# Kernel optimization log

Hardware: AMD Instinct MI355X
Metric: run time of the kernel (lower is better)

The kernel has to match this reference:

```python
import jax, jax.numpy as jnp
import numpy as np
from jax import lax

# Production-scale dims: batch, seq_len, tag_size (incl. START/STOP tags)
B, S, T = 512, 512, 64


def setup_inputs() -> dict:
    key = jax.random.key(0)
    k1, k2, k3, k4 = jax.random.split(key, 4)
    feats = jax.random.normal(k1, (B, S, T), dtype=jnp.float32)
    # prefix-contiguous mask (module assumes mask[:, 0] == 1 and length-style masks)
    lengths = jax.random.randint(k2, (B,), S // 2, S + 1)
    mask = jnp.arange(S)[None, :] < lengths[:, None]  # (B, S) bool
    tags = jax.random.randint(k3, (B, S), 0, T - 2)  # gold tags exclude START/STOP
    transitions = jax.random.normal(k4, (T, T), dtype=jnp.float32) * 0.1
    return {"feats": feats, "mask": mask, "tags": tags, "transitions": transitions}


def _crf_nll(feats, transitions, mask, tags):
    b, s, t = feats.shape
    START, STOP = t - 2, t - 1  # START_TAG = -2, STOP_TAG = -1

    # ---- forward (log partition), matches _calculate_PZ ----
    # partition init: scores[0][:, START, :] = feats[:,0,:] + transitions[START, :]
    init = feats[:, 0, :] + transitions[START][None, :]  # (b, t)

    feats_t = jnp.swapaxes(feats, 0, 1)  # (s, b, t)
    mask_t = jnp.swapaxes(mask, 0, 1)    # (s, b)

    def step(partition, inp):
        f_t, m_t = inp  # (b, t), (b,)
        # cur_values[b, from, to] = feats_t[b, to] + transitions[from, to] + partition[b, from]
        cur = partition[:, :, None] + transitions[None, :, :] + f_t[:, None, :]
        new_p = jax.nn.logsumexp(cur, axis=1)  # reduce over 'from' -> (b, t)
        partition = jnp.where(m_t[:, None], new_p, partition)
        return partition, None

    partition, _ = lax.scan(step, init, (feats_t[1:], mask_t[1:]))

    # final transition to STOP
    final = jax.nn.logsumexp(partition[:, :, None] + transitions[None, :, :], axis=1)
    forward_score = final[:, STOP].sum()

    # ---- gold score, matches _score_sentence ----
    prev = jnp.concatenate(
        [jnp.full((b, 1), START, dtype=tags.dtype), tags[:, :-1]], axis=1
    )  # (b, s): previous tag, START at position 0
    emit = jnp.take_along_axis(feats, tags[:, :, None], axis=2)[:, :, 0]  # (b, s)
    tg_energy = emit + transitions[prev, tags]  # (b, s)
    gold = jnp.where(mask, tg_energy, jnp.zeros((), feats.dtype)).sum()
    lengths = mask.sum(axis=1).astype(jnp.int32)  # (b,)
    end_ids = jnp.take_along_axis(tags, (lengths - 1)[:, None].astype(tags.dtype), axis=1)[:, 0]
    gold = gold + transitions[end_ids, STOP].sum()

    # average_batch = False
    return forward_score - gold


def reference(feats, mask, tags, transitions):
    return _crf_nll(feats, transitions, mask, tags)
```

## Files before the change

kernel.cpp:

```cpp
#include <hip/hip_runtime.h>

#define BB 512
#define SS 512
#define TT 64
#define START_TAG 62
#define STOP_TAG 63

#define LOG2E 1.4426950408889634f
#define LN2   0.6931471805599453f

typedef _Float16 h2 __attribute__((ext_vector_type(2)));
typedef _Float16 h8 __attribute__((ext_vector_type(8)));
typedef float    f4 __attribute__((ext_vector_type(4)));

__device__ __forceinline__ h2 pkrtz(float a, float b) {
    return __builtin_bit_cast(h2, __builtin_amdgcn_cvt_pkrtz(a, b));
}
__device__ __forceinline__ f4 MF(h8 a, h8 b, f4 c) {
    return __builtin_amdgcn_mfma_f32_16x16x32_f16(a, b, c, 0, 0, 0);
}

__global__ void __launch_bounds__(192) crf_main(
    const float* __restrict__ feats, const int* __restrict__ mask,
    const int* __restrict__ tags, const float* __restrict__ trans,
    float* __restrict__ out)
{
    const int b    = blockIdx.x;
    const int tid  = threadIdx.x;
    const int wv   = tid >> 6;
    const int lane = tid & 63;

    const float* frow = feats + (size_t)b * SS * TT;
    const int*   mrow = mask + b * SS;

    __shared__ __align__(16) _Float16 febuf[2][8][TT];
    __shared__ __align__(16) float xbuf[TT];
    __shared__ __align__(16) float ybuf[TT];
    __shared__ int ks_sh;

    int cnt = 0;
    #pragma unroll
    for (int s = lane; s < SS; s += 64) cnt += (mrow[s] != 0);
    #pragma unroll
    for (int off = 32; off; off >>= 1) cnt += __shfl_xor(cnt, off);
    const int len = cnt;
    const int h   = len >> 1;

    float offs = 0.f;
    int   ksum = 0;

    if (wv < 2) {
        const bool isF = (wv == 0);
        const int g  = lane >> 4;
        const int cg = lane & 15;
        const int to_base = 16 * (cg >> 2) + (cg & 3);
        const int nstep = isF ? h : (len - h - 2);
        const int base  = isF ? 1 : (len - 2);
        const int dir   = isF ? 1 : -1;
        _Float16 (*febw)[TT] = febuf[wv];

        h8 A[4][2];
        #pragma unroll
        for (int tt = 0; tt < 4; ++tt)
            #pragma unroll
            for (int kc = 0; kc < 2; ++kc)
                #pragma unroll
                for (int j = 0; j < 8; ++j) {
                    const int kt = 16 * g + 8 * kc + j;
                    const int ot = to_base + 4 * tt;
                    const int ix = isF ? (kt * TT + ot) : (ot * TT + kt);
                    A[tt][kc][j] =
                        (_Float16)__builtin_amdgcn_exp2f(trans[ix] * LOG2E);
                }

        h8 B0, B1;
        if (isF) {
            offs = frow[0] + trans[START_TAG * TT + 0];
            #pragma unroll
            for (int sl = 0; sl < 8; ++sl) {
                const int t0 = 16 * g + sl, t1 = t0 + 8;
                B0[sl] = (_Float16)__builtin_amdgcn_exp2f(
                    (frow[t0] + trans[START_TAG * TT + t0] - offs) * LOG2E);
                B1[sl] = (_Float16)__builtin_amdgcn_exp2f(
                    (frow[t1] + trans[START_TAG * TT + t1] - offs) * LOG2E);
            }
        } else {
            const float* fl = frow + (size_t)(len - 1) * TT;
            #pragma unroll
            for (int sl = 0; sl < 8; ++sl) {
                const int t0 = 16 * g + sl, t1 = t0 + 8;
                B0[sl] = (_Float16)__builtin_amdgcn_exp2f(
                    (fl[t0] + trans[t0 * TT + STOP_TAG]) * LOG2E);
                B1[sl] = (_Float16)__builtin_amdgcn_exp2f(
                    (fl[t1] + trans[t1 * TT + STOP_TAG]) * LOG2E);
            }
        }

        auto rowOf = [&](int idx) {
            int r = base + dir * idx;
            return r < 0 ? 0 : (r > SS - 1 ? SS - 1 : r);
        };

        float fr[8];
        #pragma unroll
        for (int j = 0; j < 8; ++j)
            fr[j] = frow[(size_t)rowOf(j) * TT + lane];
        #pragma unroll
        for (int j = 0; j < 4; ++j)
            febw[rowOf(j) & 7][lane] =
                (_Float16)__builtin_amdgcn_exp2f(fr[j] * LOG2E);
        h8 cL0, cL1, cL2, cL3, cH0, cH1, cH2, cH3;
        {
            const _Float16* p0 = &febw[rowOf(0) & 7][16 * g];
            const _Float16* p1 = &febw[rowOf(1) & 7][16 * g];
            const _Float16* p2 = &febw[rowOf(2) & 7][16 * g];
            const _Float16* p3 = &febw[rowOf(3) & 7][16 * g];
            cL0 = *(const h8*)p0; cH0 = *(const h8*)(p0 + 8);
            cL1 = *(const h8*)p1; cH1 = *(const h8*)(p1 + 8);
            cL2 = *(const h8*)p2; cH2 = *(const h8*)(p2 + 8);
            cL3 = *(const h8*)p3; cH3 = *(const h8*)(p3 + 8);
        }

        const f4 Z = {0.f, 0.f, 0.f, 0.f};
        auto STEP = [&](h8 feL, h8 feH) {
            f4 d0 = MF(A[0][0], B0, Z);
            f4 d1 = MF(A[1][0], B0, Z);
            f4 d2 = MF(A[2][0], B0, Z);
            f4 d3 = MF(A[3][0], B0, Z);
            d0 = MF(A[0][1], B1, d0);
            d1 = MF(A[1][1], B1, d1);
            d2 = MF(A[2][1], B1, d2);
            d3 = MF(A[3][1], B1, d3);
            const int eb = (__builtin_amdgcn_readfirstlane(
                                __float_as_int(d0[0])) >> 23) & 0xff;
            ksum += eb - 127;
            const float sc = __int_as_float((254 - eb) << 23);
            const h2 p0 = pkrtz(d0[0] * sc, d0[1] * sc);
            const h2 p1 = pkrtz(d0[2] * sc, d0[3] * sc);
            const h2 p2 = pkrtz(d1[0] * sc, d1[1] * sc);
            const h2 p3 = pkrtz(d1[2] * sc, d1[3] * sc);
            const h2 p4 = pkrtz(d2[0] * sc, d2[1] * sc);
            const h2 p5 = pkrtz(d2[2] * sc, d2[3] * sc);
            const h2 p6 = pkrtz(d3[0] * sc, d3[1] * sc);
            const h2 p7 = pkrtz(d3[2] * sc, d3[3] * sc);
            const h2 q0 = p0 * __builtin_shufflevector(feL, feL, 0, 1);
            const h2 q1 = p1 * __builtin_shufflevector(feL, feL, 2, 3);
            const h2 q2 = p2 * __builtin_shufflevector(feL, feL, 4, 5);
            const h2 q3 = p3 * __builtin_shufflevector(feL, feL, 6, 7);
            const h2 q4 = p4 * __builtin_shufflevector(feH, feH, 0, 1);
            const h2 q5 = p5 * __builtin_shufflevector(feH, feH, 2, 3);
            const h2 q6 = p6 * __builtin_shufflevector(feH, feH, 4, 5);
            const h2 q7 = p7 * __builtin_shufflevector(feH, feH, 6, 7);
            B0 = __builtin_shufflevector(
                     __builtin_shufflevector(q0, q1, 0, 1, 2, 3),
                     __builtin_shufflevector(q2, q3, 0, 1, 2, 3),
                     0, 1, 2, 3, 4, 5, 6, 7);
            B1 = __builtin_shufflevector(
                     __builtin_shufflevector(q4, q5, 0, 1, 2, 3),
                     __builtin_shufflevector(q6, q7, 0, 1, 2, 3),
                     0, 1, 2, 3, 4, 5, 6, 7);
        };

        int i = 0;
        for (; i + 3 < nstep; i += 4) {
            const float n0 = frow[(size_t)rowOf(i + 8)  * TT + lane];
            const float n1 = frow[(size_t)rowOf(i + 9)  * TT + lane];
            const float n2 = frow[(size_t)rowOf(i + 10) * TT + lane];
            const float n3 = frow[(size_t)rowOf(i + 11) * TT + lane];
            febw[rowOf(i + 4) & 7][lane] =
                (_Float16)__builtin_amdgcn_exp2f(fr[4] * LOG2E);
            febw[rowOf(i + 5) & 7][lane] =
                (_Float16)__builtin_amdgcn_exp2f(fr[5] * LOG2E);
            febw[rowOf(i + 6) & 7][lane] =
                (_Float16)__builtin_amdgcn_exp2f(fr[6] * LOG2E);
            febw[rowOf(i + 7) & 7][lane] =
                (_Float16)__builtin_amdgcn_exp2f(fr[7] * LOG2E);
            const _Float16* q0p = &febw[rowOf(i + 4) & 7][16 * g];
            const _Float16* q1p = &febw[rowOf(i + 5) & 7][16 * g];
            const _Float16* q2p = &febw[rowOf(i + 6) & 7][16 * g];
            const _Float16* q3p = &febw[rowOf(i + 7) & 7][16 * g];
            const h8 nL0 = *(const h8*)q0p, nH0 = *(const h8*)(q0p + 8);
            const h8 nL1 = *(const h8*)q1p, nH1 = *(const h8*)(q1p + 8);
            const h8 nL2 = *(const h8*)q2p, nH2 = *(const h8*)(q2p + 8);
            const h8 nL3 = *(const h8*)q3p, nH3 = *(const h8*)(q3p + 8);

            STEP(cL0, cH0); STEP(cL1, cH1); STEP(cL2, cH2); STEP(cL3, cH3);

            cL0 = nL0; cH0 = nH0; cL1 = nL1; cH1 = nH1;
            cL2 = nL2; cH2 = nH2; cL3 = nL3; cH3 = nH3;
            #pragma unroll
            for (int j = 0; j < 4; ++j) fr[j] = fr[j + 4];
            fr[4] = n0; fr[5] = n1; fr[6] = n2; fr[7] = n3;
        }

        const int rem = nstep - i;
        if (rem > 0) STEP(cL0, cH0);
        if (rem > 1) STEP(cL1, cH1);
        if (rem > 2) STEP(cL2, cH2);

        if (isF) {
            f4 d0 = MF(A[0][0], B0, Z);
            f4 d1 = MF(A[1][0], B0, Z);
            f4 d2 = MF(A[2][0], B0, Z);
            f4 d3 = MF(A[3][0], B0, Z);
            d0 = MF(A[0][1], B1, d0);
            d1 = MF(A[1][1], B1, d1);
            d2 = MF(A[2][1], B1, d2);
            d3 = MF(A[3][1], B1, d3);
            const int eb = (__builtin_amdgcn_readfirstlane(
                                __float_as_int(d0[0])) >> 23) & 0xff;
            ksum += eb - 127;
            const float sc = __int_as_float((254 - eb) << 23);
            if (cg == 0) {
                #pragma unroll
                for (int r = 0; r < 4; ++r) {
                    xbuf[16 * g + 0 * 4 + r] = d0[r] * sc;
                    xbuf[16 * g + 1 * 4 + r] = d1[r] * sc;
                    xbuf[16 * g + 2 * 4 + r] = d2[r] * sc;
                    xbuf[16 * g + 3 * 4 + r] = d3[r] * sc;
                }
            }
        } else {
            if (cg == 0) {
                #pragma unroll
                for (int sl = 0; sl < 8; ++sl) {
                    ybuf[16 * g + sl]     = (float)B0[sl];
                    ybuf[16 * g + 8 + sl] = (float)B1[sl];
                }
            }
            if (lane == 0) ks_sh = ksum;
        }
    } else {
        const int* trow = tags + b * SS;
        float acc = 0.f;
        for (int s = lane; s < SS; s += 64) {
            if (mrow[s] != 0) {
                const int tag  = trow[s];
                const int prev = (s == 0) ? START_TAG : trow[s - 1];
                acc += frow[(size_t)s * TT + tag] + trans[prev * TT + tag];
            }
        }
        #pragma unroll
        for (int off = 32; off; off >>= 1) acc += __shfl_xor(acc, off);
        if (lane == 0) {
            const int end_id = trow[len - 1];
            atomicAdd(out, -(acc + trans[end_id * TT + STOP_TAG]));
        }
    }

    __syncthreads();

    if (wv == 0) {
        float z = xbuf[lane] * ybuf[lane];
        #pragma unroll
        for (int off = 32; off; off >>= 1) z += __shfl_xor(z, off);
        if (lane == 0)
            atomicAdd(out, offs + (float)(ksum + ks_sh) * LN2
                           + LN2 * __builtin_amdgcn_logf(z));
    }
}

extern "C" void kernel_launch(void* const* d_in, const int* in_sizes, int n_in,
                              void* d_out, int out_size, void* d_ws, size_t ws_size,
                              hipStream_t stream) {
    const float* feats = (const float*)d_in[0];
    const int*   mask  = (const int*)d_in[1];
    const int*   tags  = (const int*)d_in[2];
    const float* trans = (const float*)d_in[3];
    float* out = (float*)d_out;

    (void)hipMemsetAsync(out, 0, sizeof(float), stream);
    crf_main<<<BB, 192, 0, stream>>>(feats, mask, tags, trans, out);
}
```

Before: 166.8 us.

## Split CRF recurrence into four segments using transfer-matrix products on extra waves

Sequential forward-algorithm work goes from two chains (forward and backward halves) to four segments. Two extra waves each accumulate a 64x64 product of per-step transfer matrices with MFMA for a middle segment, and the results are combined through shared memory at the end. The aim is a shorter serial critical path per block. In exchange each matrix-step costs four times the MFMAs of a vector step, occupancy per block rises to 256 threads, and a small fp32 matrix-vector epilogue is added. The per-step fp16 rescaling of the whole matrix by a single exponent risks precision loss.

Result: slower. 215.0 us (+28.9%).

```diff
diff --git a/kernel.cpp b/kernel.cpp
--- a/kernel.cpp
+++ b/kernel.cpp
@@ -20,7 +20,7 @@
     return __builtin_amdgcn_mfma_f32_16x16x32_f16(a, b, c, 0, 0, 0);
 }
 
-__global__ void __launch_bounds__(192) crf_main(
+__global__ void __launch_bounds__(256) crf_main(
     const float* __restrict__ feats, const int* __restrict__ mask,
     const int* __restrict__ tags, const float* __restrict__ trans,
     float* __restrict__ out)
@@ -29,14 +29,17 @@
     const int tid  = threadIdx.x;
     const int wv   = tid >> 6;
     const int lane = tid & 63;
+    const int g    = lane >> 4;
+    const int cg   = lane & 15;
 
     const float* frow = feats + (size_t)b * SS * TT;
     const int*   mrow = mask + b * SS;
 
-    __shared__ __align__(16) _Float16 febuf[2][8][TT];
-    __shared__ __align__(16) float xbuf[TT];
-    __shared__ __align__(16) float ybuf[TT];
-    __shared__ int ks_sh;
+    __shared__ __align__(16) _Float16 febuf[4][8][TT];
+    __shared__ __align__(16) _Float16 TAbuf[TT][TT];
+    __shared__ __align__(16) _Float16 TBbuf[TT][TT];
+    __shared__ __align__(16) float xbuf[TT], ubuf[TT], x2buf[TT];
+    __shared__ int ks_sh[4];
 
     int cnt = 0;
     #pragma unroll
@@ -44,37 +47,87 @@
     #pragma unroll
     for (int off = 32; off; off >>= 1) cnt += __shfl_xor(cnt, off);
     const int len = cnt;
-    const int h   = len >> 1;
+
+    int h1 = (len >> 2) - 9;
+    const int remt = len - 2 - h1;
+    const int mA = remt / 3, mB = remt / 3;
 
     float offs = 0.f;
     int   ksum = 0;
 
-    if (wv < 2) {
-        const bool isF = (wv == 0);
-        const int g  = lane >> 4;
-        const int cg = lane & 15;
-        const int to_base = 16 * (cg >> 2) + (cg & 3);
-        const int nstep = isF ? h : (len - h - 2);
-        const int base  = isF ? 1 : (len - 2);
-        const int dir   = isF ? 1 : -1;
-        _Float16 (*febw)[TT] = febuf[wv];
-
-        h8 A[4][2];
-        #pragma unroll
-        for (int tt = 0; tt < 4; ++tt)
-            #pragma unroll
-            for (int kc = 0; kc < 2; ++kc)
-                #pragma unroll
-                for (int j = 0; j < 8; ++j) {
-                    const int kt = 16 * g + 8 * kc + j;
-                    const int ot = to_base + 4 * tt;
-                    const int ix = isF ? (kt * TT + ot) : (ot * TT + kt);
-                    A[tt][kc][j] =
-                        (_Float16)__builtin_amdgcn_exp2f(trans[ix] * LOG2E);
-                }
-
+    if (wv == 0) {
+        const int* trow = tags + b * SS;
+        float acc = 0.f;
+        for (int s = lane; s < SS; s += 64) {
+            if (mrow[s] != 0) {
+                const int tag  = trow[s];
+                const int prev = (s == 0) ? START_TAG : trow[s - 1];
+                acc += frow[(size_t)s * TT + tag] + trans[prev * TT + tag];
+            }
+        }
+        #pragma unroll
+        for (int off = 32; off; off >>= 1) acc += __shfl_xor(acc, off);
+        if (lane == 0) {
+            const int end_id = trow[len - 1];
+            atomicAdd(out, -(acc + trans[end_id * TT + STOP_TAG]));
+        }
+    }
+
+    const bool isB   = (wv == 1);
+    const bool isMat = (wv >= 2);
+    const int nstep = (wv == 0) ? h1
+                    : (wv == 1) ? (remt - mA - mB)
+                    : (wv == 2) ? mA : mB;
+    const int base  = (wv == 0) ? 1
+                    : (wv == 1) ? (len - 2)
+                    : (wv == 2) ? (h1 + 1) : (h1 + mA + 1);
+    const int dir   = isB ? -1 : 1;
+    _Float16 (*febw)[TT] = febuf[wv];
+
+    const int to_base = 16 * (cg >> 2) + (cg & 3);
+    h8 A[4][2];
+    #pragma unroll
+    for (int tt = 0; tt < 4; ++tt)
+        #pragma unroll
+        for (int kc = 0; kc < 2; ++kc)
+            #pragma unroll
+            for (int j = 0; j < 8; ++j) {
+                const int kt = 16 * g + 8 * kc + j;
+                const int ot = to_base + 4 * tt;
+                const int ix = isB ? (ot * TT + kt) : (kt * TT + ot);
+                A[tt][kc][j] =
+                    (_Float16)__builtin_amdgcn_exp2f(trans[ix] * LOG2E);
+            }
+
+    auto rowOf = [&](int idx) {
+        int r = base + dir * idx;
+        return r < 0 ? 0 : (r > SS - 1 ? SS - 1 : r);
+    };
+
+    float fr[8];
+    #pragma unroll
+    for (int j = 0; j < 8; ++j)
+        fr[j] = frow[(size_t)rowOf(j) * TT + lane];
+    #pragma unroll
+    for (int j = 0; j < 4; ++j)
+        febw[rowOf(j) & 7][lane] =
+            (_Float16)__builtin_amdgcn_exp2f(fr[j] * LOG2E);
+    h8 cL0, cL1, cL2, cL3, cH0, cH1, cH2, cH3;
+    {
+        const _Float16* p0 = &febw[rowOf(0) & 7][16 * g];
+        const _Float16* p1 = &febw[rowOf(1) & 7][16 * g];
+        const _Float16* p2 = &febw[rowOf(2) & 7][16 * g];
+        const _Float16* p3 = &febw[rowOf(3) & 7][16 * g];
+        cL0 = *(const h8*)p0; cH0 = *(const h8*)(p0 + 8);
+        cL1 = *(const h8*)p1; cH1 = *(const h8*)(p1 + 8);
+        cL2 = *(const h8*)p2; cH2 = *(const h8*)(p2 + 8);
+        cL3 = *(const h8*)p3; cH3 = *(const h8*)(p3 + 8);
+    }
+    const f4 Zz = {0.f, 0.f, 0.f, 0.f};
+
+    if (!isMat) {
         h8 B0, B1;
-        if (isF) {
+        if (wv == 0) {
             offs = frow[0] + trans[START_TAG * TT + 0];
             #pragma unroll
             for (int sl = 0; sl < 8; ++sl) {
@@ -96,37 +149,11 @@
             }
         }
 
-        auto rowOf = [&](int idx) {
-            int r = base + dir * idx;
-            return r < 0 ? 0 : (r > SS - 1 ? SS - 1 : r);
-        };
-
-        float fr[8];
-        #pragma unroll
-        for (int j = 0; j < 8; ++j)
-            fr[j] = frow[(size_t)rowOf(j) * TT + lane];
-        #pragma unroll
-        for (int j = 0; j < 4; ++j)
-            febw[rowOf(j) & 7][lane] =
-                (_Float16)__builtin_amdgcn_exp2f(fr[j] * LOG2E);
-        h8 cL0, cL1, cL2, cL3, cH0, cH1, cH2, cH3;
-        {
-            const _Float16* p0 = &febw[rowOf(0) & 7][16 * g];
-            const _Float16* p1 = &febw[rowOf(1) & 7][16 * g];
-            const _Float16* p2 = &febw[rowOf(2) & 7][16 * g];
-            const _Float16* p3 = &febw[rowOf(3) & 7][16 * g];
-            cL0 = *(const h8*)p0; cH0 = *(const h8*)(p0 + 8);
-            cL1 = *(const h8*)p1; cH1 = *(const h8*)(p1 + 8);
-            cL2 = *(const h8*)p2; cH2 = *(const h8*)(p2 + 8);
-            cL3 = *(const h8*)p3; cH3 = *(const h8*)(p3 + 8);
-        }
-
-        const f4 Z = {0.f, 0.f, 0.f, 0.f};
         auto STEP = [&](h8 feL, h8 feH) {
-            f4 d0 = MF(A[0][0], B0, Z);
-            f4 d1 = MF(A[1][0], B0, Z);
-            f4 d2 = MF(A[2][0], B0, Z);
-            f4 d3 = MF(A[3][0], B0, Z);
+            f4 d0 = MF(A[0][0], B0, Zz);
+            f4 d1 = MF(A[1][0], B0, Zz);
+            f4 d2 = MF(A[2][0], B0, Zz);
+            f4 d3 = MF(A[3][0], B0, Zz);
             d0 = MF(A[0][1], B1, d0);
             d1 = MF(A[1][1], B1, d1);
             d2 = MF(A[2][1], B1, d2);
@@ -192,71 +219,164 @@
             for (int j = 0; j < 4; ++j) fr[j] = fr[j + 4];
             fr[4] = n0; fr[5] = n1; fr[6] = n2; fr[7] = n3;
         }
-
         const int rem = nstep - i;
         if (rem > 0) STEP(cL0, cH0);
         if (rem > 1) STEP(cL1, cH1);
         if (rem > 2) STEP(cL2, cH2);
 
-        if (isF) {
-            f4 d0 = MF(A[0][0], B0, Z);
-            f4 d1 = MF(A[1][0], B0, Z);
-            f4 d2 = MF(A[2][0], B0, Z);
-            f4 d3 = MF(A[3][0], B0, Z);
-            d0 = MF(A[0][1], B1, d0);
-            d1 = MF(A[1][1], B1, d1);
-            d2 = MF(A[2][1], B1, d2);
-            d3 = MF(A[3][1], B1, d3);
+        float* obuf = (wv == 0) ? xbuf : ubuf;
+        if (cg == 0) {
+            #pragma unroll
+            for (int sl = 0; sl < 8; ++sl) {
+                obuf[16 * g + sl]     = (float)B0[sl];
+                obuf[16 * g + 8 + sl] = (float)B1[sl];
+            }
+        }
+        if (lane == 0) ks_sh[wv] = ksum;
+    } else {
+        h8 Bt0[4], Bt1[4];
+        #pragma unroll
+        for (int ct = 0; ct < 4; ++ct)
+            #pragma unroll
+            for (int sl = 0; sl < 8; ++sl) {
+                Bt0[ct][sl] = (_Float16)((g == ct && cg == sl) ? 1.0f : 0.0f);
+                Bt1[ct][sl] = (_Float16)((g == ct && cg == sl + 8) ? 1.0f : 0.0f);
+            }
+
+        auto MSTEP = [&](h8 feL, h8 feH, bool useFe) {
+            f4 D[4][4];
+            #pragma unroll
+            for (int ct = 0; ct < 4; ++ct) {
+                D[ct][0] = MF(A[0][0], Bt0[ct], Zz);
+                D[ct][1] = MF(A[1][0], Bt0[ct], Zz);
+                D[ct][2] = MF(A[2][0], Bt0[ct], Zz);
+                D[ct][3] = MF(A[3][0], Bt0[ct], Zz);
+            }
+            #pragma unroll
+            for (int ct = 0; ct < 4; ++ct) {
+                D[ct][0] = MF(A[0][1], Bt1[ct], D[ct][0]);
+                D[ct][1] = MF(A[1][1], Bt1[ct], D[ct][1]);
+                D[ct][2] = MF(A[2][1], Bt1[ct], D[ct][2]);
+                D[ct][3] = MF(A[3][1], Bt1[ct], D[ct][3]);
+            }
             const int eb = (__builtin_amdgcn_readfirstlane(
-                                __float_as_int(d0[0])) >> 23) & 0xff;
+                                __float_as_int(D[0][0][0])) >> 23) & 0xff;
             ksum += eb - 127;
             const float sc = __int_as_float((254 - eb) << 23);
-            if (cg == 0) {
-                #pragma unroll
-                for (int r = 0; r < 4; ++r) {
-                    xbuf[16 * g + 0 * 4 + r] = d0[r] * sc;
-                    xbuf[16 * g + 1 * 4 + r] = d1[r] * sc;
-                    xbuf[16 * g + 2 * 4 + r] = d2[r] * sc;
-                    xbuf[16 * g + 3 * 4 + r] = d3[r] * sc;
+            #pragma unroll
+            for (int ct = 0; ct < 4; ++ct) {
+                h2 p0 = pkrtz(D[ct][0][0] * sc, D[ct][0][1] * sc);
+                h2 p1 = pkrtz(D[ct][0][2] * sc, D[ct][0][3] * sc);
+                h2 p2 = pkrtz(D[ct][1][0] * sc, D[ct][1][1] * sc);
+                h2 p3 = pkrtz(D[ct][1][2] * sc, D[ct][1][3] * sc);
+                h2 p4 = pkrtz(D[ct][2][0] * sc, D[ct][2][1] * sc);
+                h2 p5 = pkrtz(D[ct][2][2] * sc, D[ct][2][3] * sc);
+                h2 p6 = pkrtz(D[ct][3][0] * sc, D[ct][3][1] * sc);
+                h2 p7 = pkrtz(D[ct][3][2] * sc, D[ct][3][3] * sc);
+                if (useFe) {
+                    p0 = p0 * __builtin_shufflevector(feL, feL, 0, 1);
+                    p1 = p1 * __builtin_shufflevector(feL, feL, 2, 3);
+                    p2 = p2 * __builtin_shufflevector(feL, feL, 4, 5);
+                    p3 = p3 * __builtin_shufflevector(feL, feL, 6, 7);
+                    p4 = p4 * __builtin_shufflevector(feH, feH, 0, 1);
+                    p5 = p5 * __builtin_shufflevector(feH, feH, 2, 3);
+                    p6 = p6 * __builtin_shufflevector(feH, feH, 4, 5);
+                    p7 = p7 * __builtin_shufflevector(feH, feH, 6, 7);
                 }
-            }
-        } else {
-            if (cg == 0) {
-                #pragma unroll
-                for (int sl = 0; sl < 8; ++sl) {
-                    ybuf[16 * g + sl]     = (float)B0[sl];
-                    ybuf[16 * g + 8 + sl] = (float)B1[sl];
-                }
-            }
-            if (lane == 0) ks_sh = ksum;
-        }
-    } else {
-        const int* trow = tags + b * SS;
-        float acc = 0.f;
-        for (int s = lane; s < SS; s += 64) {
-            if (mrow[s] != 0) {
-                const int tag  = trow[s];
-                const int prev = (s == 0) ? START_TAG : trow[s - 1];
-                acc += frow[(size_t)s * TT + tag] + trans[prev * TT + tag];
-            }
-        }
-        #pragma unroll
-        for (int off = 32; off; off >>= 1) acc += __shfl_xor(acc, off);
-        if (lane == 0) {
-            const int end_id = trow[len - 1];
-            atomicAdd(out, -(acc + trans[end_id * TT + STOP_TAG]));
-        }
+                Bt0[ct] = __builtin_shufflevector(
+                              __builtin_shufflevector(p0, p1, 0, 1, 2, 3),
+                              __builtin_shufflevector(p2, p3, 0, 1, 2, 3),
+                              0, 1, 2, 3, 4, 5, 6, 7);
+                Bt1[ct] = __builtin_shufflevector(
+                              __builtin_shufflevector(p4, p5, 0, 1, 2, 3),
+                              __builtin_shufflevector(p6, p7, 0, 1, 2, 3),
+                              0, 1, 2, 3, 4, 5, 6, 7);
+            }
+        };
+
+        int i = 0;
+        for (; i + 3 < nstep; i += 4) {
+            const float n0 = frow[(size_t)rowOf(i + 8)  * TT + lane];
+            const float n1 = frow[(size_t)rowOf(i + 9)  * TT + lane];
+            const float n2 = frow[(size_t)rowOf(i + 10) * TT + lane];
+            const float n3 = frow[(size_t)rowOf(i + 11) * TT + lane];
+            febw[rowOf(i + 4) & 7][lane] =
+                (_Float16)__builtin_amdgcn_exp2f(fr[4] * LOG2E);
+            febw[rowOf(i + 5) & 7][lane] =
+                (_Float16)__builtin_amdgcn_exp2f(fr[5] * LOG2E);
+            febw[rowOf(i + 6) & 7][lane] =
+                (_Float16)__builtin_amdgcn_exp2f(fr[6] * LOG2E);
+            febw[rowOf(i + 7) & 7][lane] =
+                (_Float16)__builtin_amdgcn_exp2f(fr[7] * LOG2E);
+            const _Float16* q0p = &febw[rowOf(i + 4) & 7][16 * g];
+            const _Float16* q1p = &febw[rowOf(i + 5) & 7][16 * g];
+            const _Float16* q2p = &febw[rowOf(i + 6) & 7][16 * g];
+            const _Float16* q3p = &febw[rowOf(i + 7) & 7][16 * g];
+            const h8 nL0 = *(const h8*)q0p, nH0 = *(const h8*)(q0p + 8);
+            const h8 nL1 = *(const h8*)q1p, nH1 = *(const h8*)(q1p + 8);
+            const h8 nL2 = *(const h8*)q2p, nH2 = *(const h8*)(q2p + 8);
+            const h8 nL3 = *(const h8*)q3p, nH3 = *(const h8*)(q3p + 8);
+
+            MSTEP(cL0, cH0, true); MSTEP(cL1, cH1, true);
+            MSTEP(cL2, cH2, true); MSTEP(cL3, cH3, true);
+
+            cL0 = nL0; cH0 = nH0; cL1 = nL1; cH1 = nH1;
+            cL2 = nL2; cH2 = nH2; cL3 = nL3; cH3 = nH3;
+            #pragma unroll
+            for (int j = 0; j < 4; ++j) fr[j] = fr[j + 4];
+            fr[4] = n0; fr[5] = n1; fr[6] = n2; fr[7] = n3;
+        }
+        const int rem = nstep - i;
+        if (rem > 0) MSTEP(cL0, cH0, true);
+        if (rem > 1) MSTEP(cL1, cH1, true);
+        if (rem > 2) MSTEP(cL2, cH2, true);
+
+        if (wv == 3) MSTEP(cL0, cH0, false);
+
+        _Float16* Tb = (wv == 2) ? &TAbuf[0][0] : &TBbuf[0][0];
+        #pragma unroll
+        for (int ct = 0; ct < 4; ++ct) {
+            const int j = 16 * ct + cg;
+            #pragma unroll
+            for (int sl = 0; sl < 8; ++sl) {
+                const int i0 = 16 * g + sl, i1 = i0 + 8;
+                Tb[j * TT + ((i0 + 2 * j) & 63)] = Bt0[ct][sl];
+                Tb[j * TT + ((i1 + 2 * j) & 63)] = Bt1[ct][sl];
+            }
+        }
+        if (lane == 0) ks_sh[wv] = ksum;
     }
 
     __syncthreads();
 
     if (wv == 0) {
-        float z = xbuf[lane] * ybuf[lane];
+        float a0 = 0.f, a1 = 0.f, a2 = 0.f, a3 = 0.f;
+        #pragma unroll
+        for (int j4 = 0; j4 < 16; ++j4) {
+            const int j = 4 * j4;
+            a0 += (float)TAbuf[j + 0][(lane + 2 * (j + 0)) & 63] * xbuf[j + 0];
+            a1 += (float)TAbuf[j + 1][(lane + 2 * (j + 1)) & 63] * xbuf[j + 1];
+            a2 += (float)TAbuf[j + 2][(lane + 2 * (j + 2)) & 63] * xbuf[j + 2];
+            a3 += (float)TAbuf[j + 3][(lane + 2 * (j + 3)) & 63] * xbuf[j + 3];
+        }
+        x2buf[lane] = (a0 + a1) + (a2 + a3);
+        float c0 = 0.f, c1 = 0.f, c2 = 0.f, c3 = 0.f;
+        #pragma unroll
+        for (int j4 = 0; j4 < 16; ++j4) {
+            const int j = 4 * j4;
+            c0 += (float)TBbuf[j + 0][(lane + 2 * (j + 0)) & 63] * x2buf[j + 0];
+            c1 += (float)TBbuf[j + 1][(lane + 2 * (j + 1)) & 63] * x2buf[j + 1];
+            c2 += (float)TBbuf[j + 2][(lane + 2 * (j + 2)) & 63] * x2buf[j + 2];
+            c3 += (float)TBbuf[j + 3][(lane + 2 * (j + 3)) & 63] * x2buf[j + 3];
+        }
+        const float x3 = (c0 + c1) + (c2 + c3);
+        float z = ubuf[lane] * x3;
         #pragma unroll
         for (int off = 32; off; off >>= 1) z += __shfl_xor(z, off);
         if (lane == 0)
-            atomicAdd(out, offs + (float)(ksum + ks_sh) * LN2
-                           + LN2 * __builtin_amdgcn_logf(z));
+            atomicAdd(out, offs
+                      + (float)(ksum + ks_sh[1] + ks_sh[2] + ks_sh[3]) * LN2
+                      + LN2 * __builtin_amdgcn_logf(z));
     }
 }
 
@@ -270,5 +390,5 @@
     float* out = (float*)d_out;
 
     (void)hipMemsetAsync(out, 0, sizeof(float), stream);
-    crf_main<<<BB, 192, 0, stream>>>(feats, mask, tags, trans, out);
+    crf_main<<<BB, 256, 0, stream>>>(feats, mask, tags, trans, out);
 }
```
